# Kernel tuning notes

Measured on AMD Instinct MI355X. Metric: run time of the kernel, lower is better.

## Reference

```python
import jax, jax.numpy as jnp
import numpy as np

T = 256        # number of save/step points
BATCH = 2048   # batched trajectories
DATA = 32      # state dim (data_size)
WIDTH = 128    # MLP width
DELAYS = (1.0, 2.0)  # constant delays tau_j (all >> dt so lookups are in the past)


def setup_inputs() -> dict:
    key = jax.random.key(0)
    ks = jax.random.split(key, 5)
    ts = jnp.linspace(0.0, 10.0, T, dtype=jnp.float32)
    y0 = jax.random.normal(ks[0], (BATCH, DATA), dtype=jnp.float32)
    in_size = (len(DELAYS) + 1) * DATA  # (nb_delays + 1) * data_size

    def lin(k, o, i):
        kw, kb = jax.random.split(k)
        lim = 1.0 / np.sqrt(i)
        W = jax.random.uniform(kw, (o, i), jnp.float32, -lim, lim)
        b = jax.random.uniform(kb, (o,), jnp.float32, -lim, lim)
        return W, b

    W0, b0 = lin(ks[1], WIDTH, in_size)   # in -> width
    W1, b1 = lin(ks[2], WIDTH, WIDTH)     # hidden
    W2, b2 = lin(ks[3], WIDTH, WIDTH)     # hidden
    W3, b3 = lin(ks[4], DATA, WIDTH)      # width -> out (no activation)
    return dict(ts=ts, y0=y0, W0=W0, b0=b0, W1=W1, b1=b1, W2=W2, b2=b2, W3=W3, b3=b3)


def _mlp(x, W0, b0, W1, b1, W2, b2, W3, b3):
    # eqx.nn.MLP(depth=3, activation=relu): 4 linears, relu after hidden layers
    h = jax.nn.relu(x @ W0.T + b0)
    h = jax.nn.relu(h @ W1.T + b1)
    h = jax.nn.relu(h @ W2.T + b2)
    return h @ W3.T + b3


def _solve(ts, y0, params):
    t0 = ts[0]
    dt0 = ts[1] - ts[0]

    def lookup(buf, t):
        # linear interpolation of stored history on the uniform grid;
        # t <= t0 clips to index 0 where buf[0] == y0 (constant initial history)
        s = jnp.clip((t - t0) / dt0, 0.0, T - 1.0)
        i0 = jnp.floor(s).astype(jnp.int32)
        i1 = jnp.minimum(i0 + 1, T - 1)
        w = s - i0.astype(s.dtype)
        return (1.0 - w) * buf[i0] + w * buf[i1]

    def f(t, y, buf):
        hist = [lookup(buf, t - tau) for tau in DELAYS]
        return _mlp(jnp.concatenate([y] + hist, axis=-1), *params)

    buf0 = jnp.zeros((T, BATCH, DATA), y0.dtype).at[0].set(y0)

    def step(carry, inp):
        y, buf = carry
        i, t, t_next = inp
        dt = t_next - t
        # Bosh3 / Bogacki-Shampine stages
        k1 = f(t, y, buf)
        k2 = f(t + 0.5 * dt, y + 0.5 * dt * k1, buf)
        k3 = f(t + 0.75 * dt, y + 0.75 * dt * k2, buf)
        y_next = y + dt * (2.0 / 9.0 * k1 + 1.0 / 3.0 * k2 + 4.0 / 9.0 * k3)
        buf = buf.at[i + 1].set(y_next)
        return (y_next, buf), y_next

    xs = (jnp.arange(T - 1), ts[:-1], ts[1:])
    (_, _), ys_tail = jax.lax.scan(step, (y0, buf0), xs)
    return jnp.concatenate([y0[None], ys_tail], axis=0)  # [T, BATCH, DATA]


def reference(ts, y0, W0, b0, W1, b1, W2, b2, W3, b3):
    ys = _solve(ts, y0, (W0, b0, W1, b1, W2, b2, W3, b3))
    return ys, jnp.int32(T - 1)  # (solution.ys, num_steps)
```

## Files before the change

kernel.cpp:

```cpp
#include <hip/hip_runtime.h>

#define TT 256
#define BATCH 2048
#define DATA 32
#define WSLOTS 52

typedef __bf16 bf16x8 __attribute__((ext_vector_type(8)));
typedef float f32x4 __attribute__((ext_vector_type(4)));

#define MFMA(A, B, C) __builtin_amdgcn_mfma_f32_16x16x32_bf16((A), (B), (C), 0, 0, 0)

union bfp2 { uint2 u; __bf16 b[4]; };

__device__ __forceinline__ bf16x8 ldw8(const float* __restrict__ p) {
    float4 a = *(const float4*)p;
    float4 b = *(const float4*)(p + 4);
    bf16x8 r;
    r[0] = (__bf16)a.x; r[1] = (__bf16)a.y; r[2] = (__bf16)a.z; r[3] = (__bf16)a.w;
    r[4] = (__bf16)b.x; r[5] = (__bf16)b.y; r[6] = (__bf16)b.z; r[7] = (__bf16)b.w;
    return r;
}

__device__ __forceinline__ bf16x8 ldx(const char* base, int row, int kbyte) {
    return *(const bf16x8*)(base + row * 256 + (kbyte ^ ((row & 7) << 4)));
}

#define HID2(WF, KC, SRC, DST, BI0, BI1)                                              \
    {                                                                                 \
        bf16x8 xf[4];                                                                 \
        _Pragma("unroll") for (int kc = 0; kc < (KC); ++kc)                           \
            xf[kc] = ldx(SRC, m, kc * 64 + g * 16);                                   \
        f32x4 a0 = BI0, a1 = BI1;                                                     \
        _Pragma("unroll") for (int kc = 0; kc < (KC); ++kc) {                         \
            a0 = MFMA(WF[0][kc], xf[kc], a0);                                         \
            a1 = MFMA(WF[1][kc], xf[kc], a1);                                         \
        }                                                                             \
        bfp2 p0, p1;                                                                  \
        _Pragma("unroll") for (int j = 0; j < 4; ++j) {                               \
            p0.b[j] = (__bf16)fmaxf(a0[j], 0.0f);                                     \
            p1.b[j] = (__bf16)fmaxf(a1[j], 0.0f);                                     \
        }                                                                             \
        char* dr = (DST) + m * 256;                                                   \
        *(uint2*)(dr + ((tbB + g * 8) ^ sw)) = p0.u;                                  \
        *(uint2*)(dr + ((tbB + 32 + g * 8) ^ sw)) = p1.u;                             \
    }

#define PRELERP(TQT, XDST)                                                            \
    {                                                                                 \
        const int   dl  = wv - 2;                                                     \
        const float tau = dl ? 2.0f : 1.0f;                                           \
        float s = ((TQT) - tau - t0v) * ivd0;                                         \
        s = fminf(fmaxf(s, 0.0f), 255.0f);                                            \
        const int   i0 = (int)s;                                                      \
        const int   i1 = min(i0 + 1, TT - 1);                                         \
        const float w  = s - (float)i0;                                               \
        const char* h0p = histc + (i0 % WSLOTS) * 1152 + m * 72;                      \
        const char* h1p = histc + (i1 % WSLOTS) * 1152 + m * 72;                      \
        char* xr = (XDST) + m * 256;                                                  \
        _Pragma("unroll") for (int q = 0; q < 2; ++q) {                               \
            const int c2 = (q * 16 + g * 4) * 2;                                      \
            bfp2 pa, pb, pr;                                                          \
            pa.u = *(const uint2*)(h0p + c2);                                         \
            pb.u = *(const uint2*)(h1p + c2);                                         \
            _Pragma("unroll") for (int j = 0; j < 4; ++j) {                           \
                const float va = (float)pa.b[j];                                      \
                pr.b[j] = (__bf16)fmaf(w, (float)pb.b[j] - va, va);                   \
            }                                                                         \
            *(uint2*)(xr + ((64 + dl * 64 + c2) ^ sw)) = pr.u;                        \
        }                                                                             \
    }

#define DO_STAGE(USEK, CST, KP, KD, XSRC, XDST, TQT)                                  \
    {                                                                                 \
                      \
        bf16x8 xl1 = ldx(XSRC, m, 64 + g * 16);                                       \
        bf16x8 xl2 = ldx(XSRC, m, 128 + g * 16);                                      \
        f32x4 p0 = bias0[0], p1 = bias0[1];                                           \
        p0 = MFMA(W0f[0][1], xl1, p0); p1 = MFMA(W0f[1][1], xl1, p1);                 \
        p0 = MFMA(W0f[0][2], xl2, p0); p1 = MFMA(W0f[1][2], xl2, p1);                 \
        if (wv < 2) {                                                                 \
            bfp2 py;                                                                  \
            _Pragma("unroll") for (int j = 0; j < 4; ++j)                             \
                py.b[j] = (__bf16)((USEK) ? fmaf((CST) * dt, KP[j], y[j]) : y[j]);    \
            *(uint2*)((XSRC) + m * 256 + (cb2 ^ sw)) = py.u;                          \
        }                                                                             \
        __syncthreads();                                                              \
        {                        \
            bf16x8 xf0 = ldx(XSRC, m, g * 16);                                        \
            p0 = MFMA(W0f[0][0], xf0, p0);                                            \
            p1 = MFMA(W0f[1][0], xf0, p1);                                            \
            bfp2 q0, q1;                                                              \
            _Pragma("unroll") for (int j = 0; j < 4; ++j) {                           \
                q0.b[j] = (__bf16)fmaxf(p0[j], 0.0f);                                 \
                q1.b[j] = (__bf16)fmaxf(p1[j], 0.0f);                                 \
            }                                                                         \
            char* dr = hA + m * 256;                                                  \
            *(uint2*)(dr + ((tbB + g * 8) ^ sw)) = q0.u;                              \
            *(uint2*)(dr + ((tbB + 32 + g * 8) ^ sw)) = q1.u;                         \
        }                                                                             \
        __syncthreads();                                                              \
        HID2(W1f, 4, hA, hB, bias1[0], bias1[1])                                      \
        __syncthreads();                                                              \
        HID2(W2f, 4, hB, hA, bias2[0], bias2[1])                                      \
        __syncthreads();                                                              \
        if (wv < 2) {                                                                 \
            bf16x8 xf[4];                                                             \
            _Pragma("unroll") for (int kc = 0; kc < 4; ++kc)                          \
                xf[kc] = ldx(hA, m, kc * 64 + g * 16);                                \
            f32x4 a = bias3;                                                          \
            _Pragma("unroll") for (int kc = 0; kc < 4; ++kc)                          \
                a = MFMA(W3f[kc], xf[kc], a);                                         \
            KD = a;                                                                   \
        } else {                                                                      \
            PRELERP(TQT, XDST)                                                        \
        }                                                                             \
    }

__global__ __launch_bounds__(256, 1) void dde_pl(
    const float* __restrict__ ts, const float* __restrict__ y0,
    const float* __restrict__ W0, const float* __restrict__ b0,
    const float* __restrict__ W1, const float* __restrict__ b1,
    const float* __restrict__ W2, const float* __restrict__ b2,
    const float* __restrict__ W3, const float* __restrict__ b3,
    float* __restrict__ out)
{
    __shared__ __align__(16) unsigned short hist[WSLOTS][16][36];
    __shared__ __align__(16) char xb0[16 * 256];
    __shared__ __align__(16) char xb1[16 * 256];
    __shared__ __align__(16) char xb2[16 * 256];
    __shared__ __align__(16) char hA[16 * 256];
    __shared__ __align__(16) char hB[16 * 256];
    __shared__ float tsb[TT];

    const int tid  = threadIdx.x;
    const int lane = tid & 63;
    const int wv   = tid >> 6;
    const int m    = lane & 15;
    const int g    = lane >> 4;
    const int tbB  = wv * 64;
    const int sw   = (m & 7) << 4;
    const int cb   = wv * 16 + g * 4;
    const int cb2  = cb * 2;
    const int R0   = blockIdx.x * 16;
    char* histc = (char*)hist;

    for (int idx = tid; idx < WSLOTS * 16 * 18; idx += 256) ((unsigned*)hist)[idx] = 0u;
    for (int idx = tid; idx < TT; idx += 256) tsb[idx] = ts[idx];

    bf16x8 W0f[2][3], W1f[2][4], W2f[2][4], W3f[4];
    #pragma unroll
    for (int ti = 0; ti < 2; ++ti) {
        const int rw = (wv * 2 + ti) * 16 + m;
        #pragma unroll
        for (int kc = 0; kc < 3; ++kc) W0f[ti][kc] = ldw8(W0 + rw * 96 + kc * 32 + g * 8);
        #pragma unroll
        for (int kc = 0; kc < 4; ++kc) W1f[ti][kc] = ldw8(W1 + rw * 128 + kc * 32 + g * 8);
        #pragma unroll
        for (int kc = 0; kc < 4; ++kc) W2f[ti][kc] = ldw8(W2 + rw * 128 + kc * 32 + g * 8);
    }
    {
        const int rw3 = (wv & 1) * 16 + m;
        #pragma unroll
        for (int kc = 0; kc < 4; ++kc) W3f[kc] = ldw8(W3 + rw3 * 128 + kc * 32 + g * 8);
    }
    f32x4 bias0[2], bias1[2], bias2[2], bias3;
    #pragma unroll
    for (int ti = 0; ti < 2; ++ti) {
        bias0[ti] = *(const f32x4*)(b0 + (wv * 2 + ti) * 16 + g * 4);
        bias1[ti] = *(const f32x4*)(b1 + (wv * 2 + ti) * 16 + g * 4);
        bias2[ti] = *(const f32x4*)(b2 + (wv * 2 + ti) * 16 + g * 4);
    }
    bias3 = *(const f32x4*)(b3 + (wv & 1) * 16 + g * 4);

    __syncthreads();

    f32x4 y = {0.f, 0.f, 0.f, 0.f}, k1 = y, k2 = y, k3 = y;
    if (wv < 2) {
        float4 v = *(const float4*)(y0 + (R0 + m) * DATA + cb);
        y[0] = v.x; y[1] = v.y; y[2] = v.z; y[3] = v.w;
        bfp2 p;
        #pragma unroll
        for (int j = 0; j < 4; ++j) p.b[j] = (__bf16)y[j];
        *(uint2*)(histc + m * 72 + cb2) = p.u;
        *(float4*)(out + (R0 + m) * DATA + cb) = v;
    }
    if (blockIdx.x == 0 && tid == 0)
        out[(size_t)TT * BATCH * DATA] = 255.0f;
    __syncthreads();

    const float t0v  = tsb[0];
    const float ivd0 = 1.0f / (tsb[1] - tsb[0]);

    if (wv >= 2) {
        const float dt0 = tsb[1] - tsb[0];
        PRELERP(t0v, xb0)
        PRELERP(fmaf(0.5f, dt0, t0v), xb1)
        PRELERP(fmaf(0.75f, dt0, t0v), xb2)
    }
    __syncthreads();

    #pragma unroll 1
    for (int i = 0; i < TT - 1; ++i) {
        const float t   = tsb[i];
        const float tn  = tsb[i + 1];
        const float dt  = tn - t;
        const float tnn = tsb[min(i + 2, TT - 1)];
        const float dtn = tnn - tn;

        DO_STAGE(0, 0.0f,  k1, k1, xb0, xb2, fmaf(0.75f, dt, t))
        DO_STAGE(1, 0.5f,  k1, k2, xb1, xb0, tn)
        DO_STAGE(2, 0.75f, k2, k3, xb2, xb1, fmaf(0.5f, dtn, tn))

        if (wv < 2) {
            #pragma unroll
            for (int j = 0; j < 4; ++j) {
                const float ks = (2.0f / 9.0f) * k1[j] + (1.0f / 3.0f) * k2[j]
                               + (4.0f / 9.0f) * k3[j];
                y[j] = fmaf(dt, ks, y[j]);
            }
            bfp2 p; float4 v;
            p.b[0] = (__bf16)y[0]; p.b[1] = (__bf16)y[1];
            p.b[2] = (__bf16)y[2]; p.b[3] = (__bf16)y[3];
            v.x = y[0]; v.y = y[1]; v.z = y[2]; v.w = y[3];
            *(uint2*)(histc + ((i + 1) % WSLOTS) * 1152 + m * 72 + cb2) = p.u;
            *(float4*)(out + (size_t)(i + 1) * BATCH * DATA + (R0 + m) * DATA + cb) = v;
        }
    }
}

extern "C" void kernel_launch(void* const* d_in, const int* in_sizes, int n_in,
                              void* d_out, int out_size, void* d_ws, size_t ws_size,
                              hipStream_t stream) {
    const float* ts = (const float*)d_in[0];
    const float* y0 = (const float*)d_in[1];
    const float* W0 = (const float*)d_in[2];
    const float* b0 = (const float*)d_in[3];
    const float* W1 = (const float*)d_in[4];
    const float* b1 = (const float*)d_in[5];
    const float* W2 = (const float*)d_in[6];
    const float* b2 = (const float*)d_in[7];
    const float* W3 = (const float*)d_in[8];
    const float* b3 = (const float*)d_in[9];

    dde_pl<<<dim3(BATCH / 16), dim3(256), 0, stream>>>(
        ts, y0, W0, b0, W1, b1, W2, b2, W3, b3, (float*)d_out);
}
```

Before: 723.7 us.

## Replicate ODE state in every wave to remove a per-stage barrier

Every wave now keeps a full copy of y and the stage derivatives for its row (8 elements per lane), so the first-layer input is built in registers instead of being written to shared memory by two waves and then read by all after a barrier. The output-layer result is exchanged through a small swizzled shared buffer after one barrier. The history and delayed-input layouts change to padded 80-byte rows read with 16-byte vector loads. Net barrier count per stage is unchanged, but the y-write barrier before the first MFMA is gone. In exchange every wave does redundant Runge-Kutta arithmetic and the stage ends with an extra shared-memory round trip.

New measurement: 727.8 us. Within noise of the previous version (+0.6%).

```diff
diff --git a/kernel.cpp b/kernel.cpp
--- a/kernel.cpp
+++ b/kernel.cpp
@@ -11,6 +11,7 @@
 #define MFMA(A, B, C) __builtin_amdgcn_mfma_f32_16x16x32_bf16((A), (B), (C), 0, 0, 0)
 
 union bfp2 { uint2 u; __bf16 b[4]; };
+union bfp4 { uint4 q; bf16x8 v; __bf16 b[8]; };
 
 __device__ __forceinline__ bf16x8 ldw8(const float* __restrict__ p) {
     float4 a = *(const float4*)p;
@@ -54,69 +55,63 @@
         const int   i0 = (int)s;                                                      \
         const int   i1 = min(i0 + 1, TT - 1);                                         \
         const float w  = s - (float)i0;                                               \
-        const char* h0p = histc + (i0 % WSLOTS) * 1152 + m * 72;                      \
-        const char* h1p = histc + (i1 % WSLOTS) * 1152 + m * 72;                      \
-        char* xr = (XDST) + m * 256;                                                  \
-        _Pragma("unroll") for (int q = 0; q < 2; ++q) {                               \
-            const int c2 = (q * 16 + g * 4) * 2;                                      \
-            bfp2 pa, pb, pr;                                                          \
-            pa.u = *(const uint2*)(h0p + c2);                                         \
-            pb.u = *(const uint2*)(h1p + c2);                                         \
-            _Pragma("unroll") for (int j = 0; j < 4; ++j) {                           \
-                const float va = (float)pa.b[j];                                      \
-                pr.b[j] = (__bf16)fmaf(w, (float)pb.b[j] - va, va);                   \
-            }                                                                         \
-            *(uint2*)(xr + ((64 + dl * 64 + c2) ^ sw)) = pr.u;                        \
-        }                                                                             \
+        bfp4 pa, pb, pr;                                                              \
+        pa.v = *(const bf16x8*)(hists + (i0 % WSLOTS) * 1280 + m * 80 + g * 16);      \
+        pb.v = *(const bf16x8*)(hists + (i1 % WSLOTS) * 1280 + m * 80 + g * 16);      \
+        _Pragma("unroll") for (int e = 0; e < 8; ++e) {                               \
+            const float va = (float)pa.b[e];                                          \
+            pr.b[e] = (__bf16)fmaf(w, (float)pb.b[e] - va, va);                       \
+        }                                                                             \
+        *(bf16x8*)((XDST) + dl * 1280 + m * 80 + g * 16) = pr.v;                      \
     }
 
 #define DO_STAGE(USEK, CST, KP, KD, XSRC, XDST, TQT)                                  \
     {                                                                                 \
-                      \
-        bf16x8 xl1 = ldx(XSRC, m, 64 + g * 16);                                       \
-        bf16x8 xl2 = ldx(XSRC, m, 128 + g * 16);                                      \
-        f32x4 p0 = bias0[0], p1 = bias0[1];                                           \
-        p0 = MFMA(W0f[0][1], xl1, p0); p1 = MFMA(W0f[1][1], xl1, p1);                 \
-        p0 = MFMA(W0f[0][2], xl2, p0); p1 = MFMA(W0f[1][2], xl2, p1);                 \
-        if (wv < 2) {                                                                 \
-            bfp2 py;                                                                  \
-            _Pragma("unroll") for (int j = 0; j < 4; ++j)                             \
-                py.b[j] = (__bf16)((USEK) ? fmaf((CST) * dt, KP[j], y[j]) : y[j]);    \
-            *(uint2*)((XSRC) + m * 256 + (cb2 ^ sw)) = py.u;                          \
-        }                                                                             \
-        __syncthreads();                                                              \
-        {                        \
-            bf16x8 xf0 = ldx(XSRC, m, g * 16);                                        \
-            p0 = MFMA(W0f[0][0], xf0, p0);                                            \
-            p1 = MFMA(W0f[1][0], xf0, p1);                                            \
-            bfp2 q0, q1;                                                              \
-            _Pragma("unroll") for (int j = 0; j < 4; ++j) {                           \
-                q0.b[j] = (__bf16)fmaxf(p0[j], 0.0f);                                 \
-                q1.b[j] = (__bf16)fmaxf(p1[j], 0.0f);                                 \
-            }                                                                         \
-            char* dr = hA + m * 256;                                                  \
-            *(uint2*)(dr + ((tbB + g * 8) ^ sw)) = q0.u;                              \
-            *(uint2*)(dr + ((tbB + 32 + g * 8) ^ sw)) = q1.u;                         \
-        }                                                                             \
+            \
+        bfp4 xf0;                                                                     \
+        _Pragma("unroll") for (int e = 0; e < 8; ++e)                                 \
+            xf0.b[e] = (__bf16)((USEK) ? fmaf((CST) * dt, KP[e], y[e]) : y[e]);       \
+        bf16x8 xl1 = *(const bf16x8*)((XSRC) + m * 80 + g * 16);                      \
+        bf16x8 xl2 = *(const bf16x8*)((XSRC) + 1280 + m * 80 + g * 16);               \
+        f32x4 a0 = bias0[0], a1 = bias0[1];                                           \
+        a0 = MFMA(W0f[0][0], xf0.v, a0); a1 = MFMA(W0f[1][0], xf0.v, a1);             \
+        a0 = MFMA(W0f[0][1], xl1, a0);   a1 = MFMA(W0f[1][1], xl1, a1);               \
+        a0 = MFMA(W0f[0][2], xl2, a0);   a1 = MFMA(W0f[1][2], xl2, a1);               \
+        bfp2 p0, p1;                                                                  \
+        _Pragma("unroll") for (int j = 0; j < 4; ++j) {                               \
+            p0.b[j] = (__bf16)fmaxf(a0[j], 0.0f);                                     \
+            p1.b[j] = (__bf16)fmaxf(a1[j], 0.0f);                                     \
+        }                                                                             \
+        char* dr = hA + m * 256;                                                      \
+        *(uint2*)(dr + ((tbB + g * 8) ^ sw)) = p0.u;                                  \
+        *(uint2*)(dr + ((tbB + 32 + g * 8) ^ sw)) = p1.u;                             \
         __syncthreads();                                                              \
         HID2(W1f, 4, hA, hB, bias1[0], bias1[1])                                      \
         __syncthreads();                                                              \
         HID2(W2f, 4, hB, hA, bias2[0], bias2[1])                                      \
         __syncthreads();                                                              \
-        if (wv < 2) {                                                                 \
+        if (wv < 2) {                      \
             bf16x8 xf[4];                                                             \
             _Pragma("unroll") for (int kc = 0; kc < 4; ++kc)                          \
                 xf[kc] = ldx(hA, m, kc * 64 + g * 16);                                \
             f32x4 a = bias3;                                                          \
             _Pragma("unroll") for (int kc = 0; kc < 4; ++kc)                          \
                 a = MFMA(W3f[kc], xf[kc], a);                                         \
-            KD = a;                                                                   \
+            *(f32x4*)(kbuf + m * 128 + (((wv * 4 + g) ^ (m & 7)) << 4)) = a;          \
         } else {                                                                      \
             PRELERP(TQT, XDST)                                                        \
         }                                                                             \
-    }
-
-__global__ __launch_bounds__(256, 1) void dde_pl(
+        __syncthreads();                                                              \
+        {                           \
+            f32x4 q0 = *(const f32x4*)(kbuf + m * 128 + (((2 * g) ^ (m & 7)) << 4));  \
+            f32x4 q1 = *(const f32x4*)(kbuf + m * 128 + (((2 * g + 1) ^ (m & 7)) << 4)); \
+            _Pragma("unroll") for (int j = 0; j < 4; ++j) {                           \
+                KD[j] = q0[j]; KD[4 + j] = q1[j];                                     \
+            }                                                                         \
+        }                                                                             \
+    }
+
+__global__ __launch_bounds__(256, 1) void dde_m(
     const float* __restrict__ ts, const float* __restrict__ y0,
     const float* __restrict__ W0, const float* __restrict__ b0,
     const float* __restrict__ W1, const float* __restrict__ b1,
@@ -124,12 +119,13 @@
     const float* __restrict__ W3, const float* __restrict__ b3,
     float* __restrict__ out)
 {
-    __shared__ __align__(16) unsigned short hist[WSLOTS][16][36];
-    __shared__ __align__(16) char xb0[16 * 256];
-    __shared__ __align__(16) char xb1[16 * 256];
-    __shared__ __align__(16) char xb2[16 * 256];
+    __shared__ __align__(16) char hists[WSLOTS * 1280];
+    __shared__ __align__(16) char xb0[2 * 1280];
+    __shared__ __align__(16) char xb1[2 * 1280];
+    __shared__ __align__(16) char xb2[2 * 1280];
     __shared__ __align__(16) char hA[16 * 256];
     __shared__ __align__(16) char hB[16 * 256];
+    __shared__ __align__(16) char kbuf[16 * 128];
     __shared__ float tsb[TT];
 
     const int tid  = threadIdx.x;
@@ -139,12 +135,9 @@
     const int g    = lane >> 4;
     const int tbB  = wv * 64;
     const int sw   = (m & 7) << 4;
-    const int cb   = wv * 16 + g * 4;
-    const int cb2  = cb * 2;
     const int R0   = blockIdx.x * 16;
-    char* histc = (char*)hist;
-
-    for (int idx = tid; idx < WSLOTS * 16 * 18; idx += 256) ((unsigned*)hist)[idx] = 0u;
+
+    for (int idx = tid; idx < WSLOTS * 320; idx += 256) ((unsigned*)hists)[idx] = 0u;
     for (int idx = tid; idx < TT; idx += 256) tsb[idx] = ts[idx];
 
     bf16x8 W0f[2][3], W1f[2][4], W2f[2][4], W3f[4];
@@ -174,15 +167,22 @@
 
     __syncthreads();
 
-    f32x4 y = {0.f, 0.f, 0.f, 0.f}, k1 = y, k2 = y, k3 = y;
-    if (wv < 2) {
-        float4 v = *(const float4*)(y0 + (R0 + m) * DATA + cb);
-        y[0] = v.x; y[1] = v.y; y[2] = v.z; y[3] = v.w;
-        bfp2 p;
-        #pragma unroll
-        for (int j = 0; j < 4; ++j) p.b[j] = (__bf16)y[j];
-        *(uint2*)(histc + m * 72 + cb2) = p.u;
-        *(float4*)(out + (R0 + m) * DATA + cb) = v;
+    float y[8], k1[8], k2[8], k3[8];
+    {
+        float4 v0 = *(const float4*)(y0 + (R0 + m) * DATA + g * 8);
+        float4 v1 = *(const float4*)(y0 + (R0 + m) * DATA + g * 8 + 4);
+        y[0] = v0.x; y[1] = v0.y; y[2] = v0.z; y[3] = v0.w;
+        y[4] = v1.x; y[5] = v1.y; y[6] = v1.z; y[7] = v1.w;
+        #pragma unroll
+        for (int e = 0; e < 8; ++e) { k1[e] = 0.0f; k2[e] = 0.0f; k3[e] = 0.0f; }
+        if (wv == 0) {
+            bfp4 p;
+            #pragma unroll
+            for (int e = 0; e < 8; ++e) p.b[e] = (__bf16)y[e];
+            *(bf16x8*)(hists + m * 80 + g * 16) = p.v;
+            *(float4*)(out + (R0 + m) * DATA + g * 8) = v0;
+            *(float4*)(out + (R0 + m) * DATA + g * 8 + 4) = v1;
+        }
     }
     if (blockIdx.x == 0 && tid == 0)
         out[(size_t)TT * BATCH * DATA] = 255.0f;
@@ -211,19 +211,25 @@
         DO_STAGE(1, 0.5f,  k1, k2, xb1, xb0, tn)
         DO_STAGE(2, 0.75f, k2, k3, xb2, xb1, fmaf(0.5f, dtn, tn))
 
-        if (wv < 2) {
+        {
             #pragma unroll
-            for (int j = 0; j < 4; ++j) {
-                const float ks = (2.0f / 9.0f) * k1[j] + (1.0f / 3.0f) * k2[j]
-                               + (4.0f / 9.0f) * k3[j];
-                y[j] = fmaf(dt, ks, y[j]);
+            for (int e = 0; e < 8; ++e) {
+                const float ks = (2.0f / 9.0f) * k1[e] + (1.0f / 3.0f) * k2[e]
+                               + (4.0f / 9.0f) * k3[e];
+                y[e] = fmaf(dt, ks, y[e]);
             }
-            bfp2 p; float4 v;
-            p.b[0] = (__bf16)y[0]; p.b[1] = (__bf16)y[1];
-            p.b[2] = (__bf16)y[2]; p.b[3] = (__bf16)y[3];
-            v.x = y[0]; v.y = y[1]; v.z = y[2]; v.w = y[3];
-            *(uint2*)(histc + ((i + 1) % WSLOTS) * 1152 + m * 72 + cb2) = p.u;
-            *(float4*)(out + (size_t)(i + 1) * BATCH * DATA + (R0 + m) * DATA + cb) = v;
+            if (wv == 0) {
+                bfp4 p;
+                #pragma unroll
+                for (int e = 0; e < 8; ++e) p.b[e] = (__bf16)y[e];
+                *(bf16x8*)(hists + ((i + 1) % WSLOTS) * 1280 + m * 80 + g * 16) = p.v;
+                float4 o0, o1;
+                o0.x = y[0]; o0.y = y[1]; o0.z = y[2]; o0.w = y[3];
+                o1.x = y[4]; o1.y = y[5]; o1.z = y[6]; o1.w = y[7];
+                float* op = out + (size_t)(i + 1) * BATCH * DATA + (R0 + m) * DATA + g * 8;
+                *(float4*)op = o0;
+                *(float4*)(op + 4) = o1;
+            }
         }
     }
 }
@@ -242,6 +248,6 @@
     const float* W3 = (const float*)d_in[8];
     const float* b3 = (const float*)d_in[9];
 
-    dde_pl<<<dim3(BATCH / 16), dim3(256), 0, stream>>>(
+    dde_m<<<dim3(BATCH / 16), dim3(256), 0, stream>>>(
         ts, y0, W0, b0, W1, b1, W2, b2, W3, b3, (float*)d_out);
 }
```
